# Performance work log

Measured on AMD Instinct MI355X. Metric: run time of the kernel, lower is better.

The kernel has to match this reference:

```python
import jax, jax.numpy as jnp
import numpy as np

DIM = 1024
HEADS = 16
DIM_HEADS = DIM // HEADS  # 64
DIM_HIDDEN = DIM_HEADS * HEADS


def setup_inputs() -> dict:
    key = jax.random.key(0)
    k1, k2, k3, k4, k5 = jax.random.split(key, 5)
    b, t = 2, 2048
    x = jax.random.normal(k1, (b, t, DIM), dtype=jnp.float32)
    # torch nn.Linear weights are [out_features, in_features]
    s = DIM ** -0.5
    W_q = jax.random.normal(k2, (DIM_HIDDEN, DIM), dtype=jnp.float32) * s
    W_kv = jax.random.normal(k3, (2 * DIM_HIDDEN, DIM), dtype=jnp.float32) * s
    W_out = jax.random.normal(k4, (DIM, DIM_HIDDEN), dtype=jnp.float32) * s
    b_out = jax.random.normal(k5, (DIM,), dtype=jnp.float32) * 0.01
    return {"x": x, "W_q": W_q, "W_kv": W_kv, "W_out": W_out, "b_out": b_out}


def reference(x, W_q, W_kv, W_out, b_out):
    b, t, d = x.shape
    h, e = HEADS, DIM_HEADS
    # projections (Linear: x @ W.T)
    q = jnp.einsum('btd,fd->btf', x, W_q)
    kv = jnp.einsum('btd,fd->btf', x, W_kv)
    k, v = jnp.split(kv, 2, axis=-1)
    # split heads -> (b, h, t, e)
    split = lambda z: z.reshape(b, t, h, e).transpose(0, 2, 1, 3)
    q, k, v = split(q), split(k), split(v)
    # scaled dot-product attention; original uses exp/sum/div softmax
    scores = jnp.einsum('bhqe,bhke->bhqk', q, k) * (e ** -0.5)
    attn = jax.nn.softmax(scores, axis=-1)
    out = jnp.einsum('bhqk,bhke->bhqe', attn, v)
    out = out.transpose(0, 2, 1, 3).reshape(b, t, h * e)
    return jnp.einsum('btf,df->btd', out, W_out) + b_out
```

## Files before the change

kernel.cpp:

```cpp
#include <hip/hip_runtime.h>
#include <hip/hip_bf16.h>

#define BB   2
#define TT   2048
#define DD   1024
#define HH   16
#define EE   64
#define BT   4096

typedef __attribute__((ext_vector_type(8))) short bf16x8;
typedef __attribute__((ext_vector_type(4))) float floatx4;

__device__ __forceinline__ unsigned short f2bf(float f) {
  unsigned int x = __float_as_uint(f);
  x += 0x7fffu + ((x >> 16) & 1u);
  return (unsigned short)(x >> 16);
}
__device__ __forceinline__ unsigned int pack2u(float a, float b) {
  union { __hip_bfloat162 h; unsigned int u; } r;
  r.h = __float22bfloat162_rn(make_float2(a, b));
  return r.u;
}
__device__ __forceinline__ uint4 pack8(const float4& a, const float4& b) {
  union { uint4 u; __hip_bfloat162 h[4]; } r;
  r.h[0] = __float22bfloat162_rn(make_float2(a.x, a.y));
  r.h[1] = __float22bfloat162_rn(make_float2(a.z, a.w));
  r.h[2] = __float22bfloat162_rn(make_float2(b.x, b.y));
  r.h[3] = __float22bfloat162_rn(make_float2(b.z, b.w));
  return r.u;
}
__device__ __forceinline__ void ld16(unsigned short* lds, const unsigned short* g) {
  __builtin_amdgcn_global_load_lds(
      (const __attribute__((address_space(1))) unsigned int*)g,
      (__attribute__((address_space(3))) unsigned int*)lds, 16, 0, 0);
}

#define GX   524288
#define GWQ  131072
#define GWKV 262144
#define GWO  131072

__global__ __launch_bounds__(256) void convert_kernel(
    const float* __restrict__ X,  const float* __restrict__ Wq,
    const float* __restrict__ Wkv, const float* __restrict__ Wout,
    unsigned short* __restrict__ Xb, unsigned short* __restrict__ Wb,
    unsigned short* __restrict__ Wob) {
  int g = blockIdx.x * 256 + threadIdx.x;
  const float* src; unsigned short* dst; int gi;
  if (g < GX)                        { src = X;    dst = Xb;  gi = g; }
  else if ((g -= GX) < GWQ)          { src = Wq;   dst = Wb;  gi = g; }
  else if ((g -= GWQ) < GWKV)        { src = Wkv;  dst = Wb + (size_t)GWQ * 8; gi = g; }
  else                               { src = Wout; dst = Wob; gi = g - GWKV; }
  const float4* s4 = reinterpret_cast<const float4*>(src) + (size_t)gi * 2;
  float4 a = s4[0], b = s4[1];
  reinterpret_cast<uint4*>(dst)[gi] = pack8(a, b);
}

__global__ __launch_bounds__(256) void gemm_qkv_mfma(
    const unsigned short* __restrict__ Xb,
    const unsigned short* __restrict__ Wb,
    unsigned short* __restrict__ Qh,
    unsigned short* __restrict__ Kh,
    unsigned short* __restrict__ Vt) {
  __shared__ __align__(16) unsigned short As[128 * 64];
  __shared__ __align__(16) unsigned short Bs[128 * 64];
  const int tid  = threadIdx.x;
  const int lane = tid & 63, w = tid >> 6;
  const int wm = w >> 1, wn = w & 1;
  const int q = lane >> 4, c = lane & 15;
  const int bm0 = blockIdx.y * 128;
  const int bn0 = blockIdx.x * 128;
  const unsigned short* Ag = Xb + (size_t)bm0 * DD;
  const unsigned short* Bg = Wb + (size_t)bn0 * DD;

  floatx4 acc[4][4];
#pragma unroll
  for (int i = 0; i < 4; ++i)
#pragma unroll
    for (int j = 0; j < 4; ++j) acc[i][j] = (floatx4){0.f, 0.f, 0.f, 0.f};

  int prow[4], pch[4];
#pragma unroll
  for (int t = 0; t < 4; ++t) {
    int s = (w * 4 + t) * 64 + lane;
    prow[t] = s >> 3;
    pch[t]  = (s & 7) ^ (prow[t] & 7);
  }
  int aoff[4][2], boff[4][2];
#pragma unroll
  for (int i = 0; i < 4; ++i)
#pragma unroll
    for (int h = 0; h < 2; ++h) {
      aoff[i][h] = (wm * 64 + i * 16 + c) * 64 + (((q + h * 4) ^ (c & 7)) << 3);
      boff[i][h] = (wn * 64 + i * 16 + c) * 64 + (((q + h * 4) ^ (c & 7)) << 3);
    }

  for (int kk = 0; kk < DD; kk += 64) {
    __syncthreads();
#pragma unroll
    for (int t = 0; t < 4; ++t) {
      int i = w * 4 + t;
      ld16(&As[i * 512], &Ag[(size_t)prow[t] * DD + kk + pch[t] * 8]);
      ld16(&Bs[i * 512], &Bg[(size_t)prow[t] * DD + kk + pch[t] * 8]);
    }
    __syncthreads();
    bf16x8 af[4][2], bfr[4][2];
#pragma unroll
    for (int i = 0; i < 4; ++i)
#pragma unroll
      for (int h = 0; h < 2; ++h) {
        af[i][h]  = *reinterpret_cast<const bf16x8*>(&As[aoff[i][h]]);
        bfr[i][h] = *reinterpret_cast<const bf16x8*>(&Bs[boff[i][h]]);
      }
#pragma unroll
    for (int i = 0; i < 4; ++i)
#pragma unroll
      for (int j = 0; j < 4; ++j) {
        acc[i][j] = __builtin_amdgcn_mfma_f32_16x16x32_bf16(af[i][0], bfr[j][0], acc[i][j], 0, 0, 0);
        acc[i][j] = __builtin_amdgcn_mfma_f32_16x16x32_bf16(af[i][1], bfr[j][1], acc[i][j], 0, 0, 0);
      }
  }

  const int region = bn0 >> 10;
  const float scl = (region == 0) ? 0.125f : 1.0f;
#pragma unroll
  for (int i = 0; i < 4; ++i) {
#pragma unroll
    for (int j = 0; j < 4; ++j) {
#pragma unroll
      for (int reg = 0; reg < 4; ++reg) {
        int m = bm0 + wm * 64 + i * 16 + q * 4 + reg;
        int n = bn0 + wn * 64 + j * 16 + c;
        int nb = n & 1023;
        int h = nb >> 6, e = nb & 63;
        int b = m >> 11, t = m & 2047;
        unsigned short v = f2bf(acc[i][j][reg] * scl);
        if (region == 0)      Qh[((size_t)((b * HH + h) * TT + t)) * EE + e] = v;
        else if (region == 1) Kh[((size_t)((b * HH + h) * TT + t)) * EE + e] = v;
        else                  Vt[((size_t)(b * HH + h)) * EE * TT + (size_t)e * TT + t] = v;
      }
    }
  }
}

#define LP 72

__global__ __launch_bounds__(256) void attn_kernel(
    const unsigned short* __restrict__ Qh,
    const unsigned short* __restrict__ Kh,
    const unsigned short* __restrict__ Vtg,
    unsigned short* __restrict__ Aw) {
  __shared__ __align__(16) unsigned short Qs[64 * LP];
  __shared__ __align__(16) unsigned short Ks[64 * LP];
  __shared__ __align__(16) unsigned short Vs[64 * LP];

  const int tid  = threadIdx.x;
  const int lane = tid & 63;
  const int w    = tid >> 6;
  const int q    = lane >> 4;
  const int c    = lane & 15;
  const int rbase = w * 16;

  const int qt = blockIdx.x;
  const int bh = blockIdx.y;
  const size_t base = (size_t)bh * TT * EE;
  const unsigned short* Qp = Qh + base + (size_t)qt * 64 * EE;
  const unsigned short* Kp = Kh + base;
  const unsigned short* Vp = Vtg + base;

#pragma unroll
  for (int s = 0; s < 2; ++s) {
    int o = tid + s * 256;
    int r = o >> 3, e0 = (o & 7) << 3;
    *reinterpret_cast<uint4*>(&Qs[r * LP + e0]) =
        *reinterpret_cast<const uint4*>(&Qp[(size_t)r * EE + e0]);
  }
  __syncthreads();

  const int a_off = (rbase + c) * LP + q * 8;
  const int b_off = c * LP + q * 8;
  const bf16x8 aq0 = *reinterpret_cast<const bf16x8*>(&Qs[a_off]);
  const bf16x8 aq1 = *reinterpret_cast<const bf16x8*>(&Qs[a_off + 32]);

  float l_sum = 0.0f;
  floatx4 o_acc[4];
#pragma unroll
  for (int nt = 0; nt < 4; ++nt) o_acc[nt] = (floatx4){0.f, 0.f, 0.f, 0.f};

  for (int kt = 0; kt < TT / 64; ++kt) {
    __syncthreads();
#pragma unroll
    for (int s = 0; s < 2; ++s) {
      int o = tid + s * 256;
      int r = o >> 3, x0 = (o & 7) << 3;
      *reinterpret_cast<uint4*>(&Ks[r * LP + x0]) =
          *reinterpret_cast<const uint4*>(&Kp[(size_t)(kt * 64 + r) * EE + x0]);
      *reinterpret_cast<uint4*>(&Vs[r * LP + x0]) =
          *reinterpret_cast<const uint4*>(&Vp[(size_t)r * TT + kt * 64 + x0]);
    }
    __syncthreads();

    floatx4 sacc[4];
#pragma unroll
    for (int nt = 0; nt < 4; ++nt) {
      bf16x8 bk0 = *reinterpret_cast<const bf16x8*>(&Ks[b_off + nt * 16 * LP]);
      bf16x8 bk1 = *reinterpret_cast<const bf16x8*>(&Ks[b_off + nt * 16 * LP + 32]);
      sacc[nt] = (floatx4){0.f, 0.f, 0.f, 0.f};
      sacc[nt] = __builtin_amdgcn_mfma_f32_16x16x32_bf16(bk0, aq0, sacc[nt], 0, 0, 0);
      sacc[nt] = __builtin_amdgcn_mfma_f32_16x16x32_bf16(bk1, aq1, sacc[nt], 0, 0, 0);
    }

#pragma unroll
    for (int nt = 0; nt < 4; ++nt) {
      float p0 = __expf(sacc[nt][0]);
      float p1 = __expf(sacc[nt][1]);
      float p2 = __expf(sacc[nt][2]);
      float p3 = __expf(sacc[nt][3]);
      l_sum += (p0 + p1) + (p2 + p3);
      uint2 pk;
      pk.x = pack2u(p0, p1);
      pk.y = pack2u(p2, p3);
      *reinterpret_cast<uint2*>(&Qs[(rbase + c) * LP + nt * 16 + q * 4]) = pk;
    }
    asm volatile("s_waitcnt lgkmcnt(0)" ::: "memory");

    bf16x8 ap0 = *reinterpret_cast<const bf16x8*>(&Qs[a_off]);
    bf16x8 ap1 = *reinterpret_cast<const bf16x8*>(&Qs[a_off + 32]);
#pragma unroll
    for (int nt = 0; nt < 4; ++nt) {
      bf16x8 bv0 = *reinterpret_cast<const bf16x8*>(&Vs[b_off + nt * 16 * LP]);
      bf16x8 bv1 = *reinterpret_cast<const bf16x8*>(&Vs[b_off + nt * 16 * LP + 32]);
      o_acc[nt] = __builtin_amdgcn_mfma_f32_16x16x32_bf16(ap0, bv0, o_acc[nt], 0, 0, 0);
      o_acc[nt] = __builtin_amdgcn_mfma_f32_16x16x32_bf16(ap1, bv1, o_acc[nt], 0, 0, 0);
    }
  }

  l_sum += __shfl_xor(l_sum, 16, 64);
  l_sum += __shfl_xor(l_sum, 32, 64);
  float linv[4];
#pragma unroll
  for (int reg = 0; reg < 4; ++reg)
    linv[reg] = 1.0f / __shfl(l_sum, q * 4 + reg, 64);

  const int b = bh >> 4, h = bh & 15;
#pragma unroll
  for (int reg = 0; reg < 4; ++reg) {
    int t = qt * 64 + rbase + q * 4 + reg;
    size_t rowoff = ((size_t)(b * TT + t)) * DD + h * EE;
#pragma unroll
    for (int nt = 0; nt < 4; ++nt)
      Aw[rowoff + nt * 16 + c] = f2bf(o_acc[nt][reg] * linv[reg]);
  }
}

__global__ __launch_bounds__(256) void gemm_out_mfma(
    const unsigned short* __restrict__ A,
    const unsigned short* __restrict__ Wob,
    const float* __restrict__ bias,
    float* __restrict__ out) {
  __shared__ __align__(16) unsigned short As[128 * 64];
  __shared__ __align__(16) unsigned short Bs[64 * 64];
  const int tid  = threadIdx.x;
  const int lane = tid & 63, w = tid >> 6;
  const int wm = w >> 1, wn = w & 1;
  const int q = lane >> 4, c = lane & 15;
  const int bm0 = blockIdx.y * 128;
  const int bn0 = blockIdx.x * 64;
  const unsigned short* Ag = A + (size_t)bm0 * DD;
  const unsigned short* Bg = Wob + (size_t)bn0 * DD;

  floatx4 acc[4][2];
#pragma unroll
  for (int i = 0; i < 4; ++i)
#pragma unroll
    for (int j = 0; j < 2; ++j) acc[i][j] = (floatx4){0.f, 0.f, 0.f, 0.f};

  int parow[4], pach[4];
#pragma unroll
  for (int t = 0; t < 4; ++t) {
    int s = (w * 4 + t) * 64 + lane;
    parow[t] = s >> 3;
    pach[t]  = (s & 7) ^ (parow[t] & 7);
  }
  int pbrow[2], pbch[2];
#pragma unroll
  for (int t = 0; t < 2; ++t) {
    int s = (w * 2 + t) * 64 + lane;
    pbrow[t] = s >> 3;
    pbch[t]  = (s & 7) ^ (pbrow[t] & 7);
  }

  for (int kk = 0; kk < DD; kk += 64) {
    __syncthreads();
#pragma unroll
    for (int t = 0; t < 4; ++t)
      ld16(&As[(w * 4 + t) * 512], &Ag[(size_t)parow[t] * DD + kk + pach[t] * 8]);
#pragma unroll
    for (int t = 0; t < 2; ++t)
      ld16(&Bs[(w * 2 + t) * 512], &Bg[(size_t)pbrow[t] * DD + kk + pbch[t] * 8]);
    __syncthreads();
    bf16x8 af[4][2], bfr[2][2];
#pragma unroll
    for (int h = 0; h < 2; ++h) {
      int ksw = ((q + h * 4) ^ (c & 7)) << 3;
#pragma unroll
      for (int i = 0; i < 4; ++i)
        af[i][h] = *reinterpret_cast<const bf16x8*>(&As[(wm * 64 + i * 16 + c) * 64 + ksw]);
#pragma unroll
      for (int j = 0; j < 2; ++j)
        bfr[j][h] = *reinterpret_cast<const bf16x8*>(&Bs[(wn * 32 + j * 16 + c) * 64 + ksw]);
    }
#pragma unroll
    for (int i = 0; i < 4; ++i)
#pragma unroll
      for (int j = 0; j < 2; ++j) {
        acc[i][j] = __builtin_amdgcn_mfma_f32_16x16x32_bf16(af[i][0], bfr[j][0], acc[i][j], 0, 0, 0);
        acc[i][j] = __builtin_amdgcn_mfma_f32_16x16x32_bf16(af[i][1], bfr[j][1], acc[i][j], 0, 0, 0);
      }
  }

#pragma unroll
  for (int i = 0; i < 4; ++i) {
#pragma unroll
    for (int j = 0; j < 2; ++j) {
      int n = bn0 + wn * 32 + j * 16 + c;
      float bv = bias[n];
#pragma unroll
      for (int reg = 0; reg < 4; ++reg) {
        int m = bm0 + wm * 64 + i * 16 + q * 4 + reg;
        out[(size_t)m * DD + n] = acc[i][j][reg] + bv;
      }
    }
  }
}

extern "C" void kernel_launch(void* const* d_in, const int* in_sizes, int n_in,
                              void* d_out, int out_size, void* d_ws, size_t ws_size,
                              hipStream_t stream) {
  const float* X    = (const float*)d_in[0];
  const float* Wq   = (const float*)d_in[1];
  const float* Wkv  = (const float*)d_in[2];
  const float* Wout = (const float*)d_in[3];
  const float* bout = (const float*)d_in[4];
  float* out = (float*)d_out;

  unsigned short* Qh  = (unsigned short*)d_ws;
  unsigned short* Kh  = Qh + (size_t)BT * DD;
  unsigned short* Vt  = Kh + (size_t)BT * DD;
  unsigned short* Aw  = Vt + (size_t)BT * DD;
  unsigned short* Xb  = Aw;
  unsigned short* Wb  = Aw + (size_t)BT * DD;
  unsigned short* Wob = Wb + (size_t)3 * 1024 * DD;

  convert_kernel<<<dim3(4096), 256, 0, stream>>>(X, Wq, Wkv, Wout, Xb, Wb, Wob);
  gemm_qkv_mfma<<<dim3(24, 32), 256, 0, stream>>>(Xb, Wb, Qh, Kh, Vt);
  attn_kernel<<<dim3(32, 32), 256, 0, stream>>>(Qh, Kh, Vt, Aw);
  gemm_out_mfma<<<dim3(16, 32), 256, 0, stream>>>(Aw, Wob, bout, out);
}
```

Before: 209.6 us.

## Rewrite attention with 32x32x16 MFMA, 128-row query tiles, swizzled K/V LDS

The attention kernel now uses 32x32x16 bf16 MFMA instructions, with each wave owning 32 query rows, so a block covers 128 queries and the grid is halved. Q fragments are kept in registers loaded straight from global memory. K/V tiles go into unpadded LDS with an XOR-swizzled layout through an ld16 helper, and P is staged in a separate padded buffer. The aim is fewer MFMA issues, more reuse of each K/V tile and fewer LDS bank conflicts, at the cost of more accumulator registers and fewer blocks to fill the GPU.

```diff
diff --git a/kernel.cpp b/kernel.cpp
--- a/kernel.cpp
+++ b/kernel.cpp
@@ -10,6 +10,7 @@
 
 typedef __attribute__((ext_vector_type(8))) short bf16x8;
 typedef __attribute__((ext_vector_type(4))) float floatx4;
+typedef __attribute__((ext_vector_type(16))) float floatx16;
 
 __device__ __forceinline__ unsigned short f2bf(float f) {
   unsigned int x = __float_as_uint(f);
@@ -143,113 +144,117 @@
   }
 }
 
-#define LP 72
+#define LPP 72
 
 __global__ __launch_bounds__(256) void attn_kernel(
     const unsigned short* __restrict__ Qh,
     const unsigned short* __restrict__ Kh,
     const unsigned short* __restrict__ Vtg,
     unsigned short* __restrict__ Aw) {
-  __shared__ __align__(16) unsigned short Qs[64 * LP];
-  __shared__ __align__(16) unsigned short Ks[64 * LP];
-  __shared__ __align__(16) unsigned short Vs[64 * LP];
+  __shared__ __align__(16) unsigned short Ks[64 * 64];
+  __shared__ __align__(16) unsigned short Vs[64 * 64];
+  __shared__ __align__(16) unsigned short Ps[128 * LPP];
 
   const int tid  = threadIdx.x;
   const int lane = tid & 63;
   const int w    = tid >> 6;
-  const int q    = lane >> 4;
-  const int c    = lane & 15;
-  const int rbase = w * 16;
+  const int n31  = lane & 31;
+  const int g    = lane >> 5;
 
   const int qt = blockIdx.x;
   const int bh = blockIdx.y;
   const size_t base = (size_t)bh * TT * EE;
-  const unsigned short* Qp = Qh + base + (size_t)qt * 64 * EE;
+  const unsigned short* Qp = Qh + base + (size_t)qt * 128 * EE;
   const unsigned short* Kp = Kh + base;
   const unsigned short* Vp = Vtg + base;
 
-#pragma unroll
-  for (int s = 0; s < 2; ++s) {
-    int o = tid + s * 256;
-    int r = o >> 3, e0 = (o & 7) << 3;
-    *reinterpret_cast<uint4*>(&Qs[r * LP + e0]) =
-        *reinterpret_cast<const uint4*>(&Qp[(size_t)r * EE + e0]);
-  }
-  __syncthreads();
-
-  const int a_off = (rbase + c) * LP + q * 8;
-  const int b_off = c * LP + q * 8;
-  const bf16x8 aq0 = *reinterpret_cast<const bf16x8*>(&Qs[a_off]);
-  const bf16x8 aq1 = *reinterpret_cast<const bf16x8*>(&Qs[a_off + 32]);
+  bf16x8 qf[4];
+#pragma unroll
+  for (int kc = 0; kc < 4; ++kc)
+    qf[kc] = *reinterpret_cast<const bf16x8*>(
+        &Qp[(size_t)(w * 32 + n31) * EE + kc * 16 + g * 8]);
+
+  int srow[2], sch[2];
+#pragma unroll
+  for (int t = 0; t < 2; ++t) {
+    int s = (w * 2 + t) * 64 + lane;
+    srow[t] = s >> 3;
+    sch[t]  = (s & 7) ^ (srow[t] & 7);
+  }
 
   float l_sum = 0.0f;
-  floatx4 o_acc[4];
-#pragma unroll
-  for (int nt = 0; nt < 4; ++nt) o_acc[nt] = (floatx4){0.f, 0.f, 0.f, 0.f};
+  floatx16 o_acc[2];
+  o_acc[0] = (floatx16)(0.0f);
+  o_acc[1] = (floatx16)(0.0f);
+
+  const int prow_w = (w * 32 + n31) * LPP;
 
   for (int kt = 0; kt < TT / 64; ++kt) {
     __syncthreads();
 #pragma unroll
-    for (int s = 0; s < 2; ++s) {
-      int o = tid + s * 256;
-      int r = o >> 3, x0 = (o & 7) << 3;
-      *reinterpret_cast<uint4*>(&Ks[r * LP + x0]) =
-          *reinterpret_cast<const uint4*>(&Kp[(size_t)(kt * 64 + r) * EE + x0]);
-      *reinterpret_cast<uint4*>(&Vs[r * LP + x0]) =
-          *reinterpret_cast<const uint4*>(&Vp[(size_t)r * TT + kt * 64 + x0]);
-    }
-    __syncthreads();
-
-    floatx4 sacc[4];
-#pragma unroll
-    for (int nt = 0; nt < 4; ++nt) {
-      bf16x8 bk0 = *reinterpret_cast<const bf16x8*>(&Ks[b_off + nt * 16 * LP]);
-      bf16x8 bk1 = *reinterpret_cast<const bf16x8*>(&Ks[b_off + nt * 16 * LP + 32]);
-      sacc[nt] = (floatx4){0.f, 0.f, 0.f, 0.f};
-      sacc[nt] = __builtin_amdgcn_mfma_f32_16x16x32_bf16(bk0, aq0, sacc[nt], 0, 0, 0);
-      sacc[nt] = __builtin_amdgcn_mfma_f32_16x16x32_bf16(bk1, aq1, sacc[nt], 0, 0, 0);
-    }
-
-#pragma unroll
-    for (int nt = 0; nt < 4; ++nt) {
-      float p0 = __expf(sacc[nt][0]);
-      float p1 = __expf(sacc[nt][1]);
-      float p2 = __expf(sacc[nt][2]);
-      float p3 = __expf(sacc[nt][3]);
-      l_sum += (p0 + p1) + (p2 + p3);
-      uint2 pk;
-      pk.x = pack2u(p0, p1);
-      pk.y = pack2u(p2, p3);
-      *reinterpret_cast<uint2*>(&Qs[(rbase + c) * LP + nt * 16 + q * 4]) = pk;
+    for (int t = 0; t < 2; ++t) {
+      int i = w * 2 + t;
+      ld16(&Ks[i * 512], &Kp[(size_t)(kt * 64 + srow[t]) * EE + sch[t] * 8]);
+      ld16(&Vs[i * 512], &Vp[(size_t)srow[t] * TT + kt * 64 + sch[t] * 8]);
+    }
+    __syncthreads();
+
+    floatx16 sacc[2];
+#pragma unroll
+    for (int nt = 0; nt < 2; ++nt) {
+      sacc[nt] = (floatx16)(0.0f);
+      int krow = nt * 32 + n31;
+#pragma unroll
+      for (int kc = 0; kc < 4; ++kc) {
+        int swch = (kc * 2 + g) ^ (krow & 7);
+        bf16x8 kf = *reinterpret_cast<const bf16x8*>(&Ks[krow * 64 + swch * 8]);
+        sacc[nt] = __builtin_amdgcn_mfma_f32_32x32x16_bf16(kf, qf[kc], sacc[nt], 0, 0, 0);
+      }
+    }
+
+#pragma unroll
+    for (int nt = 0; nt < 2; ++nt) {
+#pragma unroll
+      for (int r = 0; r < 4; ++r) {
+        float p0 = __expf(sacc[nt][r * 4 + 0]);
+        float p1 = __expf(sacc[nt][r * 4 + 1]);
+        float p2 = __expf(sacc[nt][r * 4 + 2]);
+        float p3 = __expf(sacc[nt][r * 4 + 3]);
+        l_sum += (p0 + p1) + (p2 + p3);
+        uint2 pk;
+        pk.x = pack2u(p0, p1);
+        pk.y = pack2u(p2, p3);
+        *reinterpret_cast<uint2*>(&Ps[prow_w + nt * 32 + r * 8 + g * 4]) = pk;
+      }
     }
     asm volatile("s_waitcnt lgkmcnt(0)" ::: "memory");
 
-    bf16x8 ap0 = *reinterpret_cast<const bf16x8*>(&Qs[a_off]);
-    bf16x8 ap1 = *reinterpret_cast<const bf16x8*>(&Qs[a_off + 32]);
-#pragma unroll
-    for (int nt = 0; nt < 4; ++nt) {
-      bf16x8 bv0 = *reinterpret_cast<const bf16x8*>(&Vs[b_off + nt * 16 * LP]);
-      bf16x8 bv1 = *reinterpret_cast<const bf16x8*>(&Vs[b_off + nt * 16 * LP + 32]);
-      o_acc[nt] = __builtin_amdgcn_mfma_f32_16x16x32_bf16(ap0, bv0, o_acc[nt], 0, 0, 0);
-      o_acc[nt] = __builtin_amdgcn_mfma_f32_16x16x32_bf16(ap1, bv1, o_acc[nt], 0, 0, 0);
-    }
-  }
-
-  l_sum += __shfl_xor(l_sum, 16, 64);
+#pragma unroll
+    for (int kc = 0; kc < 4; ++kc) {
+      bf16x8 pf = *reinterpret_cast<const bf16x8*>(&Ps[prow_w + kc * 16 + g * 8]);
+#pragma unroll
+      for (int eh = 0; eh < 2; ++eh) {
+        int vrow = eh * 32 + n31;
+        int swch = (kc * 2 + g) ^ (vrow & 7);
+        bf16x8 vf = *reinterpret_cast<const bf16x8*>(&Vs[vrow * 64 + swch * 8]);
+        o_acc[eh] = __builtin_amdgcn_mfma_f32_32x32x16_bf16(pf, vf, o_acc[eh], 0, 0, 0);
+      }
+    }
+  }
+
   l_sum += __shfl_xor(l_sum, 32, 64);
-  float linv[4];
-#pragma unroll
-  for (int reg = 0; reg < 4; ++reg)
-    linv[reg] = 1.0f / __shfl(l_sum, q * 4 + reg, 64);
 
   const int b = bh >> 4, h = bh & 15;
 #pragma unroll
-  for (int reg = 0; reg < 4; ++reg) {
-    int t = qt * 64 + rbase + q * 4 + reg;
-    size_t rowoff = ((size_t)(b * TT + t)) * DD + h * EE;
-#pragma unroll
-    for (int nt = 0; nt < 4; ++nt)
-      Aw[rowoff + nt * 16 + c] = f2bf(o_acc[nt][reg] * linv[reg]);
+  for (int eh = 0; eh < 2; ++eh) {
+    int e = eh * 32 + n31;
+#pragma unroll
+    for (int reg = 0; reg < 16; ++reg) {
+      int qrl = (reg & 3) + 8 * (reg >> 2) + 4 * g;
+      float linv = 1.0f / __shfl(l_sum, qrl, 64);
+      int t = qt * 128 + w * 32 + qrl;
+      Aw[((size_t)(b * TT + t)) * DD + h * EE + e] = f2bf(o_acc[eh][reg] * linv);
+    }
   }
 }
 
@@ -354,6 +359,6 @@
 
   convert_kernel<<<dim3(4096), 256, 0, stream>>>(X, Wq, Wkv, Wout, Xb, Wb, Wob);
   gemm_qkv_mfma<<<dim3(24, 32), 256, 0, stream>>>(Xb, Wb, Qh, Kh, Vt);
-  attn_kernel<<<dim3(32, 32), 256, 0, stream>>>(Qh, Kh, Vt, Aw);
+  attn_kernel<<<dim3(16, 32), 256, 0, stream>>>(Qh, Kh, Vt, Aw);
   gemm_out_mfma<<<dim3(16, 32), 256, 0, stream>>>(Aw, Wob, bout, out);
 }
```

Result: faster. 200.8 us (-4.2%).
